# Kernel tuning notes

Measured on AMD Instinct MI355X. Metric: run time of the kernel, lower is better.

The kernel has to match this reference:

```python
import jax, jax.numpy as jnp
import numpy as np

N = 10000   # nodes
E = 160000  # edges
D = 32      # hidden_dim == out_dim
IN = 2      # 'pos' node features
STEPS = 3   # GatedGraphConv n_steps


def setup_inputs() -> dict:
    key = jax.random.key(0)
    ks = jax.random.split(key, 16)
    s = 0.1  # init scale
    inp = {
        "x": jax.random.normal(ks[0], (N, IN), jnp.float32),
        "src": jax.random.randint(ks[1], (E,), 0, N, jnp.int64),
        "dst": jax.random.randint(ks[2], (E,), 0, N, jnp.int64),
        # node embedding Linear(in_dim, out_dim)
        "W_emb": jax.random.normal(ks[3], (IN, D), jnp.float32) * s,
        "b_emb": jnp.zeros((D,), jnp.float32),
        # EdgeConv: he = relu(theta(h_dst - h_src) + phi(h_src))
        "W_theta": jax.random.normal(ks[4], (D, D), jnp.float32) * s,
        "b_theta": jnp.zeros((D,), jnp.float32),
        "W_phi": jax.random.normal(ks[5], (D, D), jnp.float32) * s,
        "b_phi": jnp.zeros((D,), jnp.float32),
        # edge_func: Linear(D,64) -> ReLU -> Linear(64, D*D)
        "W1": jax.random.normal(ks[6], (D, 64), jnp.float32) * s,
        "b1": jnp.zeros((64,), jnp.float32),
        "W2": jax.random.normal(ks[7], (64, D * D), jnp.float32) * s,
        "b2": jnp.zeros((D * D,), jnp.float32),
        # GRUCell (torch convention), gates stacked [r|z|n]
        "W_ih": jax.random.normal(ks[8], (D, 3 * D), jnp.float32) * s,
        "b_ih": jnp.zeros((3 * D,), jnp.float32),
        "W_hh": jax.random.normal(ks[9], (D, 3 * D), jnp.float32) * s,
        "b_hh": jnp.zeros((3 * D,), jnp.float32),
    }
    return inp


def _gru_cell(a, h, W_ih, b_ih, W_hh, b_hh):
    gi = a @ W_ih + b_ih          # [N, 3D]
    gh = h @ W_hh + b_hh          # [N, 3D]
    i_r, i_z, i_n = jnp.split(gi, 3, axis=-1)
    h_r, h_z, h_n = jnp.split(gh, 3, axis=-1)
    r = jax.nn.sigmoid(i_r + h_r)
    z = jax.nn.sigmoid(i_z + h_z)
    n = jnp.tanh(i_n + r * h_n)
    return (1.0 - z) * n + z * h


def reference(x, src, dst, W_emb, b_emb, W_theta, b_theta, W_phi, b_phi,
              W1, b1, W2, b2, W_ih, b_ih, W_hh, b_hh):
    # node embedding
    h = x @ W_emb + b_emb                              # [N, D]
    # EdgeConv edge embedding (per edge)
    hs, hd = h[src], h[dst]                            # [E, D] gathers
    he = jax.nn.relu((hd - hs) @ W_theta + b_theta + hs @ W_phi + b_phi)  # [E, D]
    # NNConv-style per-edge weight matrices
    We = (jax.nn.relu(he @ W1 + b1) @ W2 + b2).reshape(E, D, D)           # [E, D, D]
    # gated (GRU) propagation for STEPS steps
    for _ in range(STEPS):
        msg = jnp.einsum('ei,eio->eo', h[src], We)     # per-edge gather-bmm
        a = jax.ops.segment_sum(msg, dst, num_segments=N)  # scatter-add [N, D]
        h = _gru_cell(a, h, W_ih, b_ih, W_hh, b_hh)
    return h
```

## Files before the change

kernel.cpp:

```cpp
#include <hip/hip_runtime.h>
#include <hip/hip_bf16.h>

#define D 32

typedef const float* fp;
typedef unsigned short u16;
typedef unsigned int u32;

using short8 = __attribute__((ext_vector_type(8))) short;
using f32x4  = __attribute__((ext_vector_type(4))) float;

__device__ __forceinline__ float b2f(u32 lo16) { return __uint_as_float(lo16 << 16); }
__device__ __forceinline__ u16 f2b(float f) {
    u32 x = __float_as_uint(f);
    return (u16)((x + 0x7fffu + ((x >> 16) & 1u)) >> 16);
}

__global__ void k_hev(fp x, fp W_emb, fp b_emb, fp Wth, fp bth, fp Wph, fp bph,
                      fp W2, u16* __restrict__ W2f, fp b2,
                      float* __restrict__ h, u16* __restrict__ hbf,
                      float* __restrict__ u, float* __restrict__ v,
                      float* __restrict__ B, float* __restrict__ a,
                      int* __restrict__ cnt, int* __restrict__ cursor,
                      int Npad, int N) {
    __shared__ float sP[192];
    __shared__ float shh[8][D];
    __shared__ float sb2[1024];
    int tid = threadIdx.x;
    if (tid < 32) {
        int o = tid;
        float au0 = 0.f, au1 = 0.f, cu = 0.f, av0 = 0.f, av1 = 0.f, cv = 0.f;
        for (int i = 0; i < D; ++i) {
            float wt = Wth[i * D + o];
            float wd = Wph[i * D + o] - wt;
            au0 += W_emb[i] * wt;
            au1 += W_emb[D + i] * wt;
            cu  += b_emb[i] * wt;
            av0 += W_emb[i] * wd;
            av1 += W_emb[D + i] * wd;
            cv  += b_emb[i] * wd;
        }
        sP[o]       = au0;
        sP[32 + o]  = au1;
        sP[64 + o]  = cu + bth[o] + bph[o];
        sP[96 + o]  = av0;
        sP[128 + o] = av1;
        sP[160 + o] = cv;
    }
    if (blockIdx.x < 256) {
        int idx = blockIdx.x * 256 + tid;
        int T = idx >> 9, r = idx & 511, l = r >> 3, j = r & 7;
        int ko = T * 16 + (l & 15);
        int i = (l >> 4) * 8 + j;
        W2f[idx] = f2b(W2[(size_t)(ko >> 5) * 1024 + i * 32 + (ko & 31)]);
    }
    for (int i = tid; i < 1024; i += 256) sb2[i] = b2[i];
    __syncthreads();
    int t = blockIdx.x * 256 + tid;
    bool active = (t < N * D);
    int n = t >> 5, o = t & 31;
    if (active) {
        a[t] = 0.f;
        if (t < Npad) cnt[t] = 0;
        if (t < N) cursor[t] = 0;
        float x0 = x[2 * n], x1 = x[2 * n + 1];
        float hv = x0 * W_emb[o] + x1 * W_emb[D + o] + b_emb[o];
        h[t] = hv;
        hbf[t] = f2b(hv);
        shh[tid >> 5][o] = hv;
        u[t] = x0 * sP[o] + x1 * sP[32 + o] + sP[64 + o];
        v[t] = x0 * sP[96 + o] + x1 * sP[128 + o] + sP[160 + o];
    }
    __syncthreads();
    if (active) {
        int lr = tid >> 5;
        float acc = 0.f;
        #pragma unroll 8
        for (int i = 0; i < D; ++i) acc += shh[lr][i] * sb2[i * 32 + o];
        B[t] = acc;
    }
}

__global__ void k_count(const int* __restrict__ src, int* __restrict__ cnt, int E) {
    int e = blockIdx.x * 256 + threadIdx.x;
    if (e < E) atomicAdd(&cnt[src[e]], 1);
}

__global__ void k_scan(const int* __restrict__ cnt, int* __restrict__ roff,
                       int* __restrict__ toff, int* __restrict__ tilS,
                       int* __restrict__ tilB, int N) {
    __shared__ int pe[1024], pt[1024];
    int t = threadIdx.x;
    int per = (N + 1023) / 1024;
    int begin = t * per, end = min(begin + per, N);
    int se = 0, st = 0;
    for (int i = begin; i < end; ++i) { int c = cnt[i]; se += c; st += (c + 15) >> 4; }
    pe[t] = se; pt[t] = st;
    __syncthreads();
    for (int off = 1; off < 1024; off <<= 1) {
        int ve = (t >= off) ? pe[t - off] : 0;
        int vt = (t >= off) ? pt[t - off] : 0;
        __syncthreads();
        pe[t] += ve; pt[t] += vt;
        __syncthreads();
    }
    int pre_e = (t == 0) ? 0 : pe[t - 1];
    int pre_t = (t == 0) ? 0 : pt[t - 1];
    for (int i = begin; i < end; ++i) {
        int c = cnt[i];
        roff[i] = pre_e;
        toff[i] = pre_t;
        int nt2 = (c + 15) >> 4;
        for (int q = 0; q < nt2; ++q) { tilS[pre_t + q] = i; tilB[pre_t + q] = pre_e + 16 * q; }
        pre_e += c;
        pre_t += nt2;
    }
    if (t == 0) { roff[N] = pe[1023]; toff[N] = pt[1023]; }
}

__global__ void k_scatter(const int* __restrict__ src, const int* __restrict__ dst,
                          const int* __restrict__ roff, int* __restrict__ cursor,
                          int* __restrict__ ssrc, int* __restrict__ sdst, int E) {
    int e = blockIdx.x * 256 + threadIdx.x;
    if (e >= E) return;
    int s = src[e];
    int p = roff[s] + atomicAdd(&cursor[s], 1);
    ssrc[p] = s;
    sdst[p] = dst[e];
}

__global__ __launch_bounds__(256)
void k_edge2(const float* __restrict__ u, const float* __restrict__ v,
             const int* __restrict__ ssrc, const int* __restrict__ sdst,
             fp W1, fp b1, u16* __restrict__ g, int E) {
    __shared__ float sW1[D * 64];
    __shared__ float sb1[64];
    __shared__ float she[8][D];
    for (int i = threadIdx.x; i < D * 64; i += 256) sW1[i] = W1[i];
    if (threadIdx.x < 64) sb1[threadIdx.x] = b1[threadIdx.x];
    __syncthreads();
    int sub = threadIdx.x >> 5, o = threadIdx.x & 31;
    const float2* w2p = (const float2*)sW1;
    for (int e0 = blockIdx.x * 8; e0 < E; e0 += gridDim.x * 8) {
        int e = e0 + sub;
        if (e < E) {
            int s = ssrc[e], d2 = sdst[e];
            she[sub][o] = fmaxf(u[(size_t)d2 * D + o] + v[(size_t)s * D + o], 0.f);
        }
        __syncthreads();
        if (e < E) {
            float a0 = sb1[2 * o], a1 = sb1[2 * o + 1];
            #pragma unroll
            for (int i = 0; i < D; ++i) {
                float hv = she[sub][i];
                float2 w = w2p[i * 32 + o];
                a0 += hv * w.x;
                a1 += hv * w.y;
            }
            ((u32*)g)[(size_t)e * 32 + o] =
                (u32)f2b(fmaxf(a0, 0.f)) | ((u32)f2b(fmaxf(a1, 0.f)) << 16);
        }
        __syncthreads();
    }
}

__global__ __launch_bounds__(512)
void k_msgf(const u16* __restrict__ hbf, const u16* __restrict__ W2f,
            const float* __restrict__ Bv, const u32* __restrict__ g32,
            const int* __restrict__ tilS, const int* __restrict__ tilB,
            const int* __restrict__ roff, const int* __restrict__ toff,
            const int* __restrict__ sdst, float* __restrict__ a, int N) {
    __shared__ u32 sfrag[16 * 1024];
    int s0 = blockIdx.x * 16;
    int w = threadIdx.x >> 6, lp = threadIdx.x & 63;

    {
        int arow = s0 + (lp & 15);
        if (arow >= N) arow = N - 1;
        short8 afrag = *(const short8*)(hbf + (size_t)arow * 32 + (lp >> 4) * 8);
        int rbase = (lp >> 4) * 4;
        #pragma unroll
        for (int mi = 0; mi < 4; ++mi) {
            int k = w * 8 + 2 * mi;
            int kh = k >> 5;
            int kp = k & 31;
            int lt = ((kp >> 3) << 4) | (lp & 15);
            int jp = (kp & 7) >> 1;
            #pragma unroll
            for (int ot = 0; ot < 2; ++ot) {
                int T = 2 * k + ot;
                short8 bA = *(const short8*)(W2f + (size_t)T * 512 + lp * 8);
                short8 bB = *(const short8*)(W2f + (size_t)(T + 2) * 512 + lp * 8);
                f32x4 ca{0.f,0.f,0.f,0.f}, cb{0.f,0.f,0.f,0.f};
                ca = __builtin_amdgcn_mfma_f32_16x16x32_bf16(afrag, bA, ca, 0, 0, 0);
                cb = __builtin_amdgcn_mfma_f32_16x16x32_bf16(afrag, bB, cb, 0, 0, 0);
                int idx = (((kh << 1) | ot) << 8) + lt * 4 + jp;
                #pragma unroll
                for (int r = 0; r < 4; ++r)
                    sfrag[((rbase + r) << 10) + idx] =
                        (u32)f2b(ca[r]) | ((u32)f2b(cb[r]) << 16);
            }
        }
    }
    __syncthreads();

    int tbeg = toff[s0];
    int tend = toff[min(s0 + 16, N)];
    int ti = tbeg + w;
    uint4 A0c = make_uint4(0,0,0,0), A1c = A0c;
    int sC = 0, begC = 0, endC = 0;
    if (ti < tend) {
        sC = tilS[ti]; begC = tilB[ti]; endC = roff[sC + 1];
        int er = begC + (lp & 15);
        if (er < endC) {
            const uint4* gp = (const uint4*)(g32 + (size_t)er * 32);
            A0c = gp[lp >> 4];
            A1c = gp[4 + (lp >> 4)];
        }
    }
    while (ti < tend) {
        int tn = ti + 8;
        uint4 A0n = make_uint4(0,0,0,0), A1n = A0n;
        int sN = 0, begN = 0, endN = 0;
        if (tn < tend) {
            sN = tilS[tn]; begN = tilB[tn]; endN = roff[sN + 1];
            int er = begN + (lp & 15);
            if (er < endN) {
                const uint4* gp = (const uint4*)(g32 + (size_t)er * 32);
                A0n = gp[lp >> 4];
                A1n = gp[4 + (lp >> 4)];
            }
        }
        {
            union { uint4 u; short8 v; } A0, A1;
            A0.u = A0c; A1.u = A1c;
            const u32* mb = sfrag + ((sC - s0) << 10);
            union { uint4 u; short8 v; } B00, B01, B10, B11;
            B00.u = *(const uint4*)(mb + lp * 4);
            B01.u = *(const uint4*)(mb + 256 + lp * 4);
            B10.u = *(const uint4*)(mb + 512 + lp * 4);
            B11.u = *(const uint4*)(mb + 768 + lp * 4);
            f32x4 c0{0.f,0.f,0.f,0.f}, c1{0.f,0.f,0.f,0.f};
            c0 = __builtin_amdgcn_mfma_f32_16x16x32_bf16(A0.v, B00.v, c0, 0, 0, 0);
            c0 = __builtin_amdgcn_mfma_f32_16x16x32_bf16(A1.v, B10.v, c0, 0, 0, 0);
            c1 = __builtin_amdgcn_mfma_f32_16x16x32_bf16(A0.v, B01.v, c1, 0, 0, 0);
            c1 = __builtin_amdgcn_mfma_f32_16x16x32_bf16(A1.v, B11.v, c1, 0, 0, 0);
            int oc = lp & 15;
            float Bs0 = Bv[(size_t)sC * 32 + oc];
            float Bs1 = Bv[(size_t)sC * 32 + 16 + oc];
            int rb = (lp >> 4) * 4;
            #pragma unroll
            for (int r = 0; r < 4; ++r) {
                int e = begC + rb + r;
                if (e < endC) {
                    int d = sdst[e];
                    atomicAdd(&a[(size_t)d * 32 + oc],      c0[r] + Bs0);
                    atomicAdd(&a[(size_t)d * 32 + 16 + oc], c1[r] + Bs1);
                }
            }
        }
        ti = tn; sC = sN; begC = begN; endC = endN; A0c = A0n; A1c = A1n;
    }
}

__global__ __launch_bounds__(256)
void k_gru(float* __restrict__ a, const float* __restrict__ h,
           fp W_ih, fp b_ih, fp W_hh, fp b_hh, fp b2,
           float* __restrict__ hout, u16* __restrict__ hbf,
           float* __restrict__ Bout, int N) {
    __shared__ float sWi[D * 96], sWh[D * 96], sbi[96], sbh[96];
    __shared__ float sa[32][D], sh[32][D];
    __shared__ float sb2[1024];
    for (int i = threadIdx.x; i < D * 96; i += 256) { sWi[i] = W_ih[i]; sWh[i] = W_hh[i]; }
    for (int i = threadIdx.x; i < 1024; i += 256) sb2[i] = b2[i];
    if (threadIdx.x < 96) { sbi[threadIdx.x] = b_ih[threadIdx.x]; sbh[threadIdx.x] = b_hh[threadIdx.x]; }
    int n0 = blockIdx.x * 32;
    for (int i = threadIdx.x; i < 32 * D; i += 256) {
        int n = n0 + (i >> 5);
        if (n < N) {
            size_t idx = (size_t)n * D + (i & 31);
            sa[i >> 5][i & 31] = a[idx];
            sh[i >> 5][i & 31] = h[idx];
            a[idx] = 0.f;
        }
    }
    __syncthreads();
    int o = threadIdx.x & 31;
    #pragma unroll
    for (int z = 0; z < 4; ++z) {
        int sub = (threadIdx.x >> 5) + z * 8;
        int n = n0 + sub;
        if (n >= N) continue;
        float ir = sbi[o], iz = sbi[D + o], in_ = sbi[2 * D + o];
        float hr = sbh[o], hz = sbh[D + o], hn = sbh[2 * D + o];
        #pragma unroll
        for (int i = 0; i < D; ++i) {
            float av = sa[sub][i], hv = sh[sub][i];
            ir += av * sWi[i * 96 + o];
            iz += av * sWi[i * 96 + D + o];
            in_ += av * sWi[i * 96 + 2 * D + o];
            hr += hv * sWh[i * 96 + o];
            hz += hv * sWh[i * 96 + D + o];
            hn += hv * sWh[i * 96 + 2 * D + o];
        }
        float r = 1.f / (1.f + __expf(-(ir + hr)));
        float zz = 1.f / (1.f + __expf(-(iz + hz)));
        float nn = tanhf(in_ + r * hn);
        float hv2 = (1.f - zz) * nn + zz * sh[sub][o];
        size_t idx = (size_t)n * D + o;
        hout[idx] = hv2;
        hbf[idx] = f2b(hv2);
        sa[sub][o] = hv2;
    }
    __syncthreads();
    #pragma unroll
    for (int z = 0; z < 4; ++z) {
        int sub = (threadIdx.x >> 5) + z * 8;
        int n = n0 + sub;
        if (n >= N) continue;
        float acc = 0.f;
        #pragma unroll 8
        for (int i = 0; i < D; ++i) acc += sa[sub][i] * sb2[i * 32 + o];
        Bout[(size_t)n * D + o] = acc;
    }
}

extern "C" void kernel_launch(void* const* d_in, const int* in_sizes, int n_in,
                              void* d_out, int out_size, void* d_ws, size_t ws_size,
                              hipStream_t stream) {
    fp x      = (fp)d_in[0];
    const int* src = (const int*)d_in[1];
    const int* dst = (const int*)d_in[2];
    fp W_emb  = (fp)d_in[3];
    fp b_emb  = (fp)d_in[4];
    fp W_th   = (fp)d_in[5];
    fp b_th   = (fp)d_in[6];
    fp W_ph   = (fp)d_in[7];
    fp b_ph   = (fp)d_in[8];
    fp W1     = (fp)d_in[9];
    fp b1     = (fp)d_in[10];
    fp W2     = (fp)d_in[11];
    fp b2     = (fp)d_in[12];
    fp W_ih   = (fp)d_in[13];
    fp b_ih   = (fp)d_in[14];
    fp W_hh   = (fp)d_in[15];
    fp b_hh   = (fp)d_in[16];

    const int N = in_sizes[0] / 2;
    const int E = in_sizes[1];
    const int Npad = N + 4 - (N % 4);
    const int maxTiles = N + (E + 15) / 16;

    float* a      = (float*)d_ws;
    int*   cnt    = (int*)(a + (size_t)N * D);
    int*   cursor = cnt + Npad;
    int*   roff   = cursor + N;
    int*   toff   = roff + Npad;
    int*   ssrc   = toff + Npad;
    int*   sdst   = ssrc + E;
    int*   tilS   = sdst + E;
    int*   tilB   = tilS + maxTiles;
    float* hA     = (float*)(tilB + maxTiles);
    float* hB     = hA + (size_t)N * D;
    u16*   g      = (u16*)(hB + (size_t)N * D);
    u16*   hbf    = g + (size_t)E * 64;
    u16*   W2f    = hbf + (size_t)N * D;
    float* u      = (float*)(W2f + 65536);
    float* v      = u + (size_t)N * D;
    float* B      = v + (size_t)N * D;

    int ndBlocks = (N * D + 255) / 256;
    int eBlocks  = (E + 255) / 256;

    k_hev<<<ndBlocks, 256, 0, stream>>>(x, W_emb, b_emb, W_th, b_th, W_ph, b_ph,
                                        W2, W2f, b2, hA, hbf, u, v, B,
                                        a, cnt, cursor, Npad, N);
    k_count<<<eBlocks, 256, 0, stream>>>(src, cnt, E);
    k_scan<<<1, 1024, 0, stream>>>(cnt, roff, toff, tilS, tilB, N);
    k_scatter<<<eBlocks, 256, 0, stream>>>(src, dst, roff, cursor, ssrc, sdst, E);
    k_edge2<<<2048, 256, 0, stream>>>(u, v, ssrc, sdst, W1, b1, g, E);

    int fBlocks = (N + 15) / 16;
    float* hc = hA;
    float* hn_ = hB;
    for (int step = 0; step < 3; ++step) {
        k_msgf<<<fBlocks, 512, 0, stream>>>(hbf, W2f, B, (const u32*)g, tilS, tilB,
                                            roff, toff, sdst, a, N);
        float* dstbuf = (step == 2) ? (float*)d_out : hn_;
        k_gru<<<(N + 31) / 32, 256, 0, stream>>>(a, hc, W_ih, b_ih, W_hh, b_hh, b2,
                                                 dstbuf, hbf, B, N);
        float* t = hc; hc = hn_; hn_ = t;
    }
}
```

Baseline: 241.4 us.

## Replace block barriers with wave-local sync in edge MLP; prefetch bias in msg kernel

k_edge2 now uses 512-thread blocks where each 64-lane wave owns a private pair of edge rows in shared memory. Block-wide __syncthreads are replaced with an lgkmcnt wait and a scheduling barrier, so waves no longer stall on one another. In k_msgf the per-source bias values are loaded one tile ahead together with the g fragments, and the MFMA sequence is wrapped in s_setprio. This relies on wave-synchronous LDS behaviour being correct without a barrier.

```diff
diff --git a/kernel.cpp b/kernel.cpp
--- a/kernel.cpp
+++ b/kernel.cpp
@@ -129,38 +129,44 @@
     sdst[p] = dst[e];
 }
 
-__global__ __launch_bounds__(256)
+__global__ __launch_bounds__(512)
 void k_edge2(const float* __restrict__ u, const float* __restrict__ v,
              const int* __restrict__ ssrc, const int* __restrict__ sdst,
              fp W1, fp b1, u16* __restrict__ g, int E) {
     __shared__ float sW1[D * 64];
     __shared__ float sb1[64];
-    __shared__ float she[8][D];
-    for (int i = threadIdx.x; i < D * 64; i += 256) sW1[i] = W1[i];
+    __shared__ float she[8][2][D];
+    for (int i = threadIdx.x; i < D * 64; i += 512) sW1[i] = W1[i];
     if (threadIdx.x < 64) sb1[threadIdx.x] = b1[threadIdx.x];
     __syncthreads();
-    int sub = threadIdx.x >> 5, o = threadIdx.x & 31;
+    int w = threadIdx.x >> 6, lane = threadIdx.x & 63;
+    int sub = lane >> 5, o = lane & 31;
+    int gw = blockIdx.x * 8 + w;
+    int stride = gridDim.x * 16;
     const float2* w2p = (const float2*)sW1;
-    for (int e0 = blockIdx.x * 8; e0 < E; e0 += gridDim.x * 8) {
+    for (int e0 = gw * 2; e0 < E; e0 += stride) {
         int e = e0 + sub;
-        if (e < E) {
+        bool val = (e < E);
+        if (val) {
             int s = ssrc[e], d2 = sdst[e];
-            she[sub][o] = fmaxf(u[(size_t)d2 * D + o] + v[(size_t)s * D + o], 0.f);
-        }
-        __syncthreads();
-        if (e < E) {
+            she[w][sub][o] = fmaxf(u[(size_t)d2 * D + o] + v[(size_t)s * D + o], 0.f);
+        }
+        asm volatile("s_waitcnt lgkmcnt(0)" ::: "memory");
+        __builtin_amdgcn_sched_barrier(0);
+        if (val) {
             float a0 = sb1[2 * o], a1 = sb1[2 * o + 1];
             #pragma unroll
             for (int i = 0; i < D; ++i) {
-                float hv = she[sub][i];
-                float2 w = w2p[i * 32 + o];
-                a0 += hv * w.x;
-                a1 += hv * w.y;
+                float hv = she[w][sub][i];
+                float2 ww = w2p[i * 32 + o];
+                a0 += hv * ww.x;
+                a1 += hv * ww.y;
             }
             ((u32*)g)[(size_t)e * 32 + o] =
                 (u32)f2b(fmaxf(a0, 0.f)) | ((u32)f2b(fmaxf(a1, 0.f)) << 16);
         }
-        __syncthreads();
+        asm volatile("s_waitcnt lgkmcnt(0)" ::: "memory");
+        __builtin_amdgcn_sched_barrier(0);
     }
 }
 
@@ -204,13 +210,17 @@
     }
     __syncthreads();
 
+    int oc = lp & 15;
     int tbeg = toff[s0];
     int tend = toff[min(s0 + 16, N)];
     int ti = tbeg + w;
     uint4 A0c = make_uint4(0,0,0,0), A1c = A0c;
     int sC = 0, begC = 0, endC = 0;
+    float Bs0c = 0.f, Bs1c = 0.f;
     if (ti < tend) {
         sC = tilS[ti]; begC = tilB[ti]; endC = roff[sC + 1];
+        Bs0c = Bv[(size_t)sC * 32 + oc];
+        Bs1c = Bv[(size_t)sC * 32 + 16 + oc];
         int er = begC + (lp & 15);
         if (er < endC) {
             const uint4* gp = (const uint4*)(g32 + (size_t)er * 32);
@@ -222,8 +232,11 @@
         int tn = ti + 8;
         uint4 A0n = make_uint4(0,0,0,0), A1n = A0n;
         int sN = 0, begN = 0, endN = 0;
+        float Bs0n = 0.f, Bs1n = 0.f;
         if (tn < tend) {
             sN = tilS[tn]; begN = tilB[tn]; endN = roff[sN + 1];
+            Bs0n = Bv[(size_t)sN * 32 + oc];
+            Bs1n = Bv[(size_t)sN * 32 + 16 + oc];
             int er = begN + (lp & 15);
             if (er < endN) {
                 const uint4* gp = (const uint4*)(g32 + (size_t)er * 32);
@@ -241,25 +254,25 @@
             B10.u = *(const uint4*)(mb + 512 + lp * 4);
             B11.u = *(const uint4*)(mb + 768 + lp * 4);
             f32x4 c0{0.f,0.f,0.f,0.f}, c1{0.f,0.f,0.f,0.f};
+            __builtin_amdgcn_s_setprio(1);
             c0 = __builtin_amdgcn_mfma_f32_16x16x32_bf16(A0.v, B00.v, c0, 0, 0, 0);
             c0 = __builtin_amdgcn_mfma_f32_16x16x32_bf16(A1.v, B10.v, c0, 0, 0, 0);
             c1 = __builtin_amdgcn_mfma_f32_16x16x32_bf16(A0.v, B01.v, c1, 0, 0, 0);
             c1 = __builtin_amdgcn_mfma_f32_16x16x32_bf16(A1.v, B11.v, c1, 0, 0, 0);
-            int oc = lp & 15;
-            float Bs0 = Bv[(size_t)sC * 32 + oc];
-            float Bs1 = Bv[(size_t)sC * 32 + 16 + oc];
+            __builtin_amdgcn_s_setprio(0);
             int rb = (lp >> 4) * 4;
             #pragma unroll
             for (int r = 0; r < 4; ++r) {
                 int e = begC + rb + r;
                 if (e < endC) {
                     int d = sdst[e];
-                    atomicAdd(&a[(size_t)d * 32 + oc],      c0[r] + Bs0);
-                    atomicAdd(&a[(size_t)d * 32 + 16 + oc], c1[r] + Bs1);
+                    atomicAdd(&a[(size_t)d * 32 + oc],      c0[r] + Bs0c);
+                    atomicAdd(&a[(size_t)d * 32 + 16 + oc], c1[r] + Bs1c);
                 }
             }
         }
-        ti = tn; sC = sN; begC = begN; endC = endN; A0c = A0n; A1c = A1n;
+        ti = tn; sC = sN; begC = begN; endC = endN;
+        A0c = A0n; A1c = A1n; Bs0c = Bs0n; Bs1c = Bs1n;
     }
 }
 
@@ -378,7 +391,7 @@
     k_count<<<eBlocks, 256, 0, stream>>>(src, cnt, E);
     k_scan<<<1, 1024, 0, stream>>>(cnt, roff, toff, tilS, tilB, N);
     k_scatter<<<eBlocks, 256, 0, stream>>>(src, dst, roff, cursor, ssrc, sdst, E);
-    k_edge2<<<2048, 256, 0, stream>>>(u, v, ssrc, sdst, W1, b1, g, E);
+    k_edge2<<<2048, 512, 0, stream>>>(u, v, ssrc, sdst, W1, b1, g, E);
 
     int fBlocks = (N + 15) / 16;
     float* hc = hA;
```

After: 238.7 us. Within noise of the previous version (-1.1%).
